# Kernel optimization log

Hardware: AMD Instinct MI355X
Metric: run time of the kernel (lower is better)

The kernel has to match this reference:

```python
import jax, jax.numpy as jnp
import numpy as np

N = 10000      # nodes
F_IN = 256     # input feature dim
H1 = 128       # hidden_dim1
H2 = 64        # hidden_dim2 (latent)
E = 320000     # edges (avg degree 32)


def setup_inputs() -> dict:
    key = jax.random.key(0)
    ks = jax.random.split(key, 10)
    x = jax.random.normal(ks[0], (N, F_IN), dtype=jnp.float32)
    edge_index = jax.random.randint(ks[1], (2, E), 0, N, dtype=jnp.int64)
    edge_weight = jax.random.uniform(ks[2], (E,), dtype=jnp.float32)
    s1 = 1.0 / np.sqrt(F_IN)
    s2 = 1.0 / np.sqrt(H1)
    W1 = jax.random.normal(ks[3], (F_IN, H1), dtype=jnp.float32) * s1
    b1 = jnp.zeros((H1,), dtype=jnp.float32)
    W2 = jax.random.normal(ks[4], (H1, H2), dtype=jnp.float32) * s2
    b2 = jnp.zeros((H2,), dtype=jnp.float32)
    W3 = jax.random.normal(ks[5], (H1, H2), dtype=jnp.float32) * s2
    b3 = jnp.zeros((H2,), dtype=jnp.float32)
    return {"x": x, "edge_index": edge_index, "edge_weight": edge_weight,
            "W1": W1, "b1": b1, "W2": W2, "b2": b2, "W3": W3, "b3": b3}


def _gcn_norm(edge_index, edge_weight, n):
    # add self-loops with weight 1, symmetric deg^-1/2 normalization (PyG GCNConv)
    loop = jnp.arange(n)
    row = jnp.concatenate([edge_index[0], loop])
    col = jnp.concatenate([edge_index[1], loop])
    w = jnp.concatenate([edge_weight, jnp.ones((n,), edge_weight.dtype)])
    deg = jax.ops.segment_sum(w, col, num_segments=n)
    dis = jnp.where(deg > 0, jax.lax.rsqrt(deg), 0.0)
    norm = dis[row] * w * dis[col]
    return row, col, norm


def _gcn_conv(h, W, b, row, col, norm, n):
    hw = h @ W                                   # [N, out] transform first (PyG order)
    out = jax.ops.segment_sum(norm[:, None] * hw[row], col, num_segments=n)
    return out + b


def reference(x, edge_index, edge_weight, W1, b1, W2, b2, W3, b3):
    n = x.shape[0]
    row, col, norm = _gcn_norm(edge_index, edge_weight, n)
    h1 = jax.nn.relu(_gcn_conv(x, W1, b1, row, col, norm, n))
    mu = _gcn_conv(h1, W2, b2, row, col, norm, n)
    logvar = _gcn_conv(h1, W3, b3, row, col, norm, n)
    # eval mode: reparameterize -> mu, dropout inactive, decoder act = identity
    z = mu
    adj = z @ z.T                                # [N, N] inner-product decode
    return adj, mu, logvar
```

## Files before the change

kernel.cpp:

```cpp
#include <hip/hip_runtime.h>

#define N_NODES 10000
#define F_IN    256
#define H1      128
#define H2      64
#define NEDGE   320000
#define M_TOT   (NEDGE + N_NODES)

typedef __attribute__((ext_vector_type(8))) short          s16v8;
typedef __attribute__((ext_vector_type(8))) unsigned short u16v8;
typedef __attribute__((ext_vector_type(4))) float          f32v4;


__global__ void k_init(float* deg, int* cnt) {
    int i = blockIdx.x * blockDim.x + threadIdx.x;
    if (i < N_NODES) { deg[i] = 1.0f; cnt[i] = 1; }
}

__global__ void k_count(const int* __restrict__ ei, const float* __restrict__ w,
                        float* deg, int* cnt) {
    int e = blockIdx.x * blockDim.x + threadIdx.x;
    if (e < NEDGE) {
        int c = ei[NEDGE + e];
        atomicAdd(&deg[c], w[e]);
        atomicAdd(&cnt[c], 1);
    }
}

__global__ void k_scan(const int* __restrict__ cnt, int* __restrict__ ptr,
                       int* __restrict__ cur) {
    __shared__ int part[1024];
    int t = threadIdx.x;
    int base = t * 10;
    int local[10];
    int s = 0;
#pragma unroll
    for (int j = 0; j < 10; j++) {
        int idx = base + j;
        int v = (idx < N_NODES) ? cnt[idx] : 0;
        local[j] = s;
        s += v;
    }
    part[t] = s;
    __syncthreads();
    for (int off = 1; off < 1024; off <<= 1) {
        int v = (t >= off) ? part[t - off] : 0;
        __syncthreads();
        part[t] += v;
        __syncthreads();
    }
    int excl = t ? part[t - 1] : 0;
#pragma unroll
    for (int j = 0; j < 10; j++) {
        int idx = base + j;
        if (idx < N_NODES) {
            int p = excl + local[j];
            ptr[idx] = p;
            cur[idx] = p;
        }
    }
    if (t == 1023) ptr[N_NODES] = part[1023];
}

__global__ void k_scatter(const int* __restrict__ ei, const float* __restrict__ w,
                          const float* __restrict__ deg, int* cur,
                          int* __restrict__ src, float* __restrict__ wgt) {
    int t = blockIdx.x * blockDim.x + threadIdx.x;
    if (t >= M_TOT) return;
    int r, c; float nw;
    if (t < NEDGE) {
        r = ei[t];
        c = ei[NEDGE + t];
        nw = rsqrtf(deg[r]) * w[t] * rsqrtf(deg[c]);
    } else {
        r = c = t - NEDGE;
        float d = rsqrtf(deg[r]);
        nw = d * d;
    }
    int pos = atomicAdd(&cur[c], 1);
    src[pos] = r;
    wgt[pos] = nw;
}


__global__ __launch_bounds__(128) void k_gemm1(const float* __restrict__ x,
                                               const float* __restrict__ W1,
                                               float* __restrict__ hw) {
    __shared__ float xs[8 * F_IN];
    int i0 = blockIdx.x * 8;
    int t = threadIdx.x;
    const float4* xsrc = (const float4*)(x + (size_t)i0 * F_IN);
    float4* xd = (float4*)xs;
#pragma unroll
    for (int j = 0; j < 4; j++) xd[t + j * 128] = xsrc[t + j * 128];
    __syncthreads();
    float acc[8] = {0, 0, 0, 0, 0, 0, 0, 0};
    for (int k = 0; k < F_IN; k += 4) {
        float w0 = W1[(k + 0) * H1 + t];
        float w1 = W1[(k + 1) * H1 + t];
        float w2 = W1[(k + 2) * H1 + t];
        float w3 = W1[(k + 3) * H1 + t];
#pragma unroll
        for (int r = 0; r < 8; r++) {
            float4 xv = *(const float4*)&xs[r * F_IN + k];
            acc[r] += xv.x * w0 + xv.y * w1 + xv.z * w2 + xv.w * w3;
        }
    }
#pragma unroll
    for (int r = 0; r < 8; r++) hw[(size_t)(i0 + r) * H1 + t] = acc[r];
}

__global__ __launch_bounds__(128) void k_gemm23(const float* __restrict__ h1,
                                                const float* __restrict__ W2,
                                                const float* __restrict__ W3,
                                                float* __restrict__ t2,
                                                float* __restrict__ t3) {
    __shared__ float hs[8 * H1];
    int i0 = blockIdx.x * 8;
    int t = threadIdx.x;
    const float4* hsrc = (const float4*)(h1 + (size_t)i0 * H1);
    float4* hd = (float4*)hs;
#pragma unroll
    for (int j = 0; j < 2; j++) hd[t + j * 128] = hsrc[t + j * 128];
    __syncthreads();
    int f = t & 63;
    int sel = t >> 6;
    const float* W = sel ? W3 : W2;
    float acc[8] = {0, 0, 0, 0, 0, 0, 0, 0};
    for (int k = 0; k < H1; k += 4) {
        float w0 = W[(k + 0) * H2 + f];
        float w1 = W[(k + 1) * H2 + f];
        float w2 = W[(k + 2) * H2 + f];
        float w3 = W[(k + 3) * H2 + f];
#pragma unroll
        for (int r = 0; r < 8; r++) {
            float4 hv = *(const float4*)&hs[r * H1 + k];
            acc[r] += hv.x * w0 + hv.y * w1 + hv.z * w2 + hv.w * w3;
        }
    }
    float* o = sel ? t3 : t2;
#pragma unroll
    for (int r = 0; r < 8; r++) o[(size_t)(i0 + r) * H2 + f] = acc[r];
}


__global__ __launch_bounds__(128) void k_agg1(const int* __restrict__ ptr,
                                              const int* __restrict__ src,
                                              const float* __restrict__ wgt,
                                              const float* __restrict__ hw,
                                              const float* __restrict__ b1,
                                              float* __restrict__ h1) {
    int i = blockIdx.x;
    int f = threadIdx.x;
    int jb = ptr[i], je = ptr[i + 1];
    float acc = b1[f];
    for (int j = jb; j < je; j++)
        acc += wgt[j] * hw[(size_t)src[j] * H1 + f];
    h1[(size_t)i * H1 + f] = fmaxf(acc, 0.0f);
}

__global__ __launch_bounds__(128) void k_agg2(const int* __restrict__ ptr,
                                              const int* __restrict__ src,
                                              const float* __restrict__ wgt,
                                              const float* __restrict__ t2,
                                              const float* __restrict__ t3,
                                              const float* __restrict__ b2,
                                              const float* __restrict__ b3,
                                              float* __restrict__ mu,
                                              float* __restrict__ lv) {
    int i = blockIdx.x;
    int t = threadIdx.x;
    int f = t & 63;
    int sel = t >> 6;
    const float* tin = sel ? t3 : t2;
    float acc = sel ? b3[f] : b2[f];
    int jb = ptr[i], je = ptr[i + 1];
    for (int j = jb; j < je; j++)
        acc += wgt[j] * tin[(size_t)src[j] * H2 + f];
    float* o = sel ? lv : mu;
    o[(size_t)i * H2 + f] = acc;
}

__global__ __launch_bounds__(256, 1) void k_adj(const float* __restrict__ z,
                                                float* __restrict__ adj) {
    __shared__ __align__(16) unsigned short Ap[3][128 * 32];
    __shared__ __align__(16) unsigned short Bp[3][128 * 32];
    int tid = threadIdx.x;
    int rowBase = blockIdx.y * 128, colBase = blockIdx.x * 128;

    int lane = tid & 63;
    int wv   = tid >> 6;
    int wr = (wv >> 1) * 64;
    int wc = (wv & 1) * 64;
    int lrow = lane & 15;
    int lk   = lane >> 4;

    int sr   = tid & 127;
    int isB  = tid >> 7;
    int gbase = (isB ? colBase : rowBase) + sr;
    bool ok = gbase < N_NODES;
    const float* srcp = z + (size_t)gbase * 64;
    unsigned short* P0 = isB ? Bp[0] : Ap[0];
    unsigned short* P1 = isB ? Bp[1] : Ap[1];
    unsigned short* P2 = isB ? Bp[2] : Ap[2];

    auto stage = [&](int s) {
#pragma unroll
        for (int g = 0; g < 4; g++) {
            float v[8];
            if (ok) {
                float4 a = *(const float4*)(srcp + s * 32 + g * 8);
                float4 b = *(const float4*)(srcp + s * 32 + g * 8 + 4);
                v[0] = a.x; v[1] = a.y; v[2] = a.z; v[3] = a.w;
                v[4] = b.x; v[5] = b.y; v[6] = b.z; v[7] = b.w;
            } else {
#pragma unroll
                for (int q = 0; q < 8; q++) v[q] = 0.0f;
            }
            u16v8 hv, mv, lv8;
#pragma unroll
            for (int q = 0; q < 8; q++) {
                float xv = v[q];
                unsigned hu = __float_as_uint(xv) & 0xffff0000u;
                float r1 = xv - __uint_as_float(hu);
                unsigned mu2 = __float_as_uint(r1) & 0xffff0000u;
                float r2 = r1 - __uint_as_float(mu2);
                unsigned lu = __float_as_uint(r2) & 0xffff0000u;
                hv[q]  = (unsigned short)(hu >> 16);
                mv[q]  = (unsigned short)(mu2 >> 16);
                lv8[q] = (unsigned short)(lu >> 16);
            }
            int c = g ^ ((sr >> 1) & 3);
            int idx = sr * 32 + c * 8;
            *reinterpret_cast<u16v8*>(P0 + idx) = hv;
            *reinterpret_cast<u16v8*>(P1 + idx) = mv;
            *reinterpret_cast<u16v8*>(P2 + idx) = lv8;
        }
    };

    f32v4 acc[4][4];
#pragma unroll
    for (int i = 0; i < 4; i++)
#pragma unroll
        for (int j = 0; j < 4; j++) acc[i][j] = (f32v4)0.0f;

    s16v8 a0[4], a1[4], a2[4], b0[4], b1[4], b2[4];

#define LOADFRAGS()                                                        \
    {                                                                      \
        _Pragma("unroll")                                                  \
        for (int fq = 0; fq < 4; fq++) {                                   \
            int ra = wr + fq * 16 + lrow;                                  \
            int ca = lk ^ ((ra >> 1) & 3);                                 \
            int ia = ra * 32 + ca * 8;                                     \
            a0[fq] = *reinterpret_cast<const s16v8*>(&Ap[0][ia]);          \
            a1[fq] = *reinterpret_cast<const s16v8*>(&Ap[1][ia]);          \
            a2[fq] = *reinterpret_cast<const s16v8*>(&Ap[2][ia]);          \
            int rb = wc + fq * 16 + lrow;                                  \
            int cb = lk ^ ((rb >> 1) & 3);                                 \
            int ib = rb * 32 + cb * 8;                                     \
            b0[fq] = *reinterpret_cast<const s16v8*>(&Bp[0][ib]);          \
            b1[fq] = *reinterpret_cast<const s16v8*>(&Bp[1][ib]);          \
            b2[fq] = *reinterpret_cast<const s16v8*>(&Bp[2][ib]);          \
        }                                                                  \
    }

#define MFMAS()                                                            \
    {                                                                      \
        _Pragma("unroll")                                                  \
        for (int i = 0; i < 4; i++) {                                      \
            _Pragma("unroll")                                              \
            for (int j = 0; j < 4; j++) {                                  \
                f32v4 c = acc[i][j];                                       \
                c = __builtin_amdgcn_mfma_f32_16x16x32_bf16(a0[i], b0[j], c, 0, 0, 0); \
                c = __builtin_amdgcn_mfma_f32_16x16x32_bf16(a0[i], b1[j], c, 0, 0, 0); \
                c = __builtin_amdgcn_mfma_f32_16x16x32_bf16(a1[i], b0[j], c, 0, 0, 0); \
                c = __builtin_amdgcn_mfma_f32_16x16x32_bf16(a0[i], b2[j], c, 0, 0, 0); \
                c = __builtin_amdgcn_mfma_f32_16x16x32_bf16(a2[i], b0[j], c, 0, 0, 0); \
                c = __builtin_amdgcn_mfma_f32_16x16x32_bf16(a1[i], b1[j], c, 0, 0, 0); \
                acc[i][j] = c;                                             \
            }                                                              \
        }                                                                  \
    }

    stage(0);
    __syncthreads();
    LOADFRAGS();
    __syncthreads();
    stage(1);
    MFMAS();
    __syncthreads();
    LOADFRAGS();
    MFMAS();

#undef LOADFRAGS
#undef MFMAS

#pragma unroll
    for (int i = 0; i < 4; i++) {
        int r0 = rowBase + wr + i * 16 + lk * 4;
#pragma unroll
        for (int j = 0; j < 4; j++) {
            int cg = colBase + wc + j * 16 + lrow;
            if (cg < N_NODES) {
#pragma unroll
                for (int v = 0; v < 4; v++) {
                    int rg = r0 + v;
                    if (rg < N_NODES)
                        adj[(size_t)rg * N_NODES + cg] = acc[i][j][v];
                }
            }
        }
    }
}


extern "C" void kernel_launch(void* const* d_in, const int* in_sizes, int n_in,
                              void* d_out, int out_size, void* d_ws, size_t ws_size,
                              hipStream_t stream) {
    const float* x  = (const float*)d_in[0];
    const int*   ei = (const int*)d_in[1];
    const float* w  = (const float*)d_in[2];
    const float* W1 = (const float*)d_in[3];
    const float* b1 = (const float*)d_in[4];
    const float* W2 = (const float*)d_in[5];
    const float* b2 = (const float*)d_in[6];
    const float* W3 = (const float*)d_in[7];
    const float* b3 = (const float*)d_in[8];

    float* out = (float*)d_out;
    float* adj = out;
    float* mu  = out + (size_t)N_NODES * N_NODES;
    float* lv  = mu + (size_t)N_NODES * H2;

    float* ws  = out + 80000000;
    float* deg = ws;
    int*   cnt = (int*)(ws + 10240);
    int*   ptr = (int*)(ws + 20480);
    int*   cur = (int*)(ws + 30720);
    int*   src = (int*)(ws + 40960);
    float* wgt = ws + 371200;
    float* hw  = ws + 701440;
    float* h1  = ws + 1981440;
    float* t2  = ws + 3261440;
    float* t3  = ws + 3901440;

    hipLaunchKernelGGL(k_init,    dim3((N_NODES + 255) / 256), dim3(256), 0, stream, deg, cnt);
    hipLaunchKernelGGL(k_count,   dim3((NEDGE + 255) / 256),   dim3(256), 0, stream, ei, w, deg, cnt);
    hipLaunchKernelGGL(k_scan,    dim3(1), dim3(1024), 0, stream, cnt, ptr, cur);
    hipLaunchKernelGGL(k_scatter, dim3((M_TOT + 255) / 256),   dim3(256), 0, stream, ei, w, deg, cur, src, wgt);
    hipLaunchKernelGGL(k_gemm1,   dim3(N_NODES / 8),  dim3(128), 0, stream, x, W1, hw);
    hipLaunchKernelGGL(k_agg1,    dim3(N_NODES),      dim3(128), 0, stream, ptr, src, wgt, hw, b1, h1);
    hipLaunchKernelGGL(k_gemm23,  dim3(N_NODES / 8),  dim3(128), 0, stream, h1, W2, W3, t2, t3);
    hipLaunchKernelGGL(k_agg2,    dim3(N_NODES),      dim3(128), 0, stream, ptr, src, wgt, t2, t3, b2, b3, mu, lv);

    dim3 g((N_NODES + 127) / 128, (N_NODES + 127) / 128);
    hipLaunchKernelGGL(k_adj, g, dim3(256), 0, stream, mu, adj);
}
```

Baseline: 666.8 us.

## Exploit symmetry of z·zᵀ by computing only upper-triangle tiles

The decoder kernel now skips tiles below the diagonal, since z·zᵀ is symmetric. Each off-diagonal tile also writes its result transposed, as float4 stores into the mirrored position. This roughly halves the MFMA work and the staging of z for the adjacency matrix. The shared-memory layout is rearranged into hi/mid/lo bf16 planes of 64 columns with an XOR swizzle over 8 chunks. The mirrored stores are strided across rows, so they are less coalesced than the original row-major writes.

```diff
diff --git a/kernel.cpp b/kernel.cpp
--- a/kernel.cpp
+++ b/kernel.cpp
@@ -183,10 +183,13 @@
 
 __global__ __launch_bounds__(256, 1) void k_adj(const float* __restrict__ z,
                                                 float* __restrict__ adj) {
-    __shared__ __align__(16) unsigned short Ap[3][128 * 32];
-    __shared__ __align__(16) unsigned short Bp[3][128 * 32];
+    if (blockIdx.x < blockIdx.y) return;
+    __shared__ __align__(16) unsigned short PAs[128 * 64];
+    __shared__ __align__(16) unsigned short PBs[128 * 64];
+    __shared__ __align__(16) unsigned short PLs[128 * 64];
     int tid = threadIdx.x;
     int rowBase = blockIdx.y * 128, colBase = blockIdx.x * 128;
+    bool diag = (blockIdx.x == blockIdx.y);
 
     int lane = tid & 63;
     int wv   = tid >> 6;
@@ -200,9 +203,9 @@
     int gbase = (isB ? colBase : rowBase) + sr;
     bool ok = gbase < N_NODES;
     const float* srcp = z + (size_t)gbase * 64;
-    unsigned short* P0 = isB ? Bp[0] : Ap[0];
-    unsigned short* P1 = isB ? Bp[1] : Ap[1];
-    unsigned short* P2 = isB ? Bp[2] : Ap[2];
+    unsigned short* PH = isB ? PBs : PAs;
+    int lslotBase = isB ? 4 : 0;
+    int rb7 = sr & 7;
 
     auto stage = [&](int s) {
 #pragma unroll
@@ -230,11 +233,10 @@
                 mv[q]  = (unsigned short)(mu2 >> 16);
                 lv8[q] = (unsigned short)(lu >> 16);
             }
-            int c = g ^ ((sr >> 1) & 3);
-            int idx = sr * 32 + c * 8;
-            *reinterpret_cast<u16v8*>(P0 + idx) = hv;
-            *reinterpret_cast<u16v8*>(P1 + idx) = mv;
-            *reinterpret_cast<u16v8*>(P2 + idx) = lv8;
+            int base = sr * 64;
+            *reinterpret_cast<u16v8*>(PH  + base + (( g            ^ rb7) * 8)) = hv;
+            *reinterpret_cast<u16v8*>(PH  + base + (((4 + g)       ^ rb7) * 8)) = mv;
+            *reinterpret_cast<u16v8*>(PLs + base + (((lslotBase+g) ^ rb7) * 8)) = lv8;
         }
     };
 
@@ -251,17 +253,17 @@
         _Pragma("unroll")                                                  \
         for (int fq = 0; fq < 4; fq++) {                                   \
             int ra = wr + fq * 16 + lrow;                                  \
-            int ca = lk ^ ((ra >> 1) & 3);                                 \
-            int ia = ra * 32 + ca * 8;                                     \
-            a0[fq] = *reinterpret_cast<const s16v8*>(&Ap[0][ia]);          \
-            a1[fq] = *reinterpret_cast<const s16v8*>(&Ap[1][ia]);          \
-            a2[fq] = *reinterpret_cast<const s16v8*>(&Ap[2][ia]);          \
+            int r7 = ra & 7;                                               \
+            int ia = ra * 64;                                              \
+            a0[fq] = *reinterpret_cast<const s16v8*>(&PAs[ia + ((lk       ^ r7) * 8)]); \
+            a1[fq] = *reinterpret_cast<const s16v8*>(&PAs[ia + (((4 + lk) ^ r7) * 8)]); \
+            a2[fq] = *reinterpret_cast<const s16v8*>(&PLs[ia + ((lk       ^ r7) * 8)]); \
             int rb = wc + fq * 16 + lrow;                                  \
-            int cb = lk ^ ((rb >> 1) & 3);                                 \
-            int ib = rb * 32 + cb * 8;                                     \
-            b0[fq] = *reinterpret_cast<const s16v8*>(&Bp[0][ib]);          \
-            b1[fq] = *reinterpret_cast<const s16v8*>(&Bp[1][ib]);          \
-            b2[fq] = *reinterpret_cast<const s16v8*>(&Bp[2][ib]);          \
+            int q7 = rb & 7;                                               \
+            int ib = rb * 64;                                              \
+            b0[fq] = *reinterpret_cast<const s16v8*>(&PBs[ib + ((lk       ^ q7) * 8)]); \
+            b1[fq] = *reinterpret_cast<const s16v8*>(&PBs[ib + (((4 + lk) ^ q7) * 8)]); \
+            b2[fq] = *reinterpret_cast<const s16v8*>(&PLs[ib + (((4 + lk) ^ q7) * 8)]); \
         }                                                                  \
     }
 
@@ -309,6 +311,9 @@
                     if (rg < N_NODES)
                         adj[(size_t)rg * N_NODES + cg] = acc[i][j][v];
                 }
+                if (!diag)
+                    *(float4*)&adj[(size_t)cg * N_NODES + r0] =
+                        make_float4(acc[i][j][0], acc[i][j][1], acc[i][j][2], acc[i][j][3]);
             }
         }
     }
```

Result: no change. 677.6 us (+1.6%).
